# Performance work log

Measured on AMD Instinct MI355X. Metric: run time of the kernel, lower is better.

## Reference

```python
import jax, jax.numpy as jnp
import numpy as np
import math

VOCAB = 50257
BLOCK = 2048
NE = 768


def setup_inputs() -> dict:
    key = jax.random.key(0)
    ks = jax.random.split(key, 12)
    s = 0.02
    idx = jax.random.randint(ks[0], (4, 2048), 0, VOCAB, dtype=jnp.int64 if jax.config.jax_enable_x64 else jnp.int32)
    tok_emb = jax.random.normal(ks[1], (VOCAB, NE), jnp.float32) * s
    pos_emb = jax.random.normal(ks[2], (BLOCK, NE), jnp.float32) * s
    Wk = jax.random.normal(ks[3], (NE, NE), jnp.float32) * s
    bk = jnp.zeros((NE,), jnp.float32)
    Wq = jax.random.normal(ks[4], (NE, NE), jnp.float32) * s
    bq = jnp.zeros((NE,), jnp.float32)
    Wv = jax.random.normal(ks[5], (NE, NE), jnp.float32) * s
    bv = jnp.zeros((NE,), jnp.float32)
    ln_g = jnp.ones((NE,), jnp.float32)
    ln_b = jnp.zeros((NE,), jnp.float32)
    Wh = jax.random.normal(ks[6], (NE, VOCAB), jnp.float32) * s
    bh = jnp.zeros((VOCAB,), jnp.float32)
    return {"idx": idx, "tok_emb": tok_emb, "pos_emb": pos_emb, "Wq": Wq, "bq": bq,
            "Wk": Wk, "bk": bk, "Wv": Wv, "bv": bv, "ln_g": ln_g, "ln_b": ln_b,
            "Wh": Wh, "bh": bh}


def reference(idx, tok_emb, pos_emb, Wq, bq, Wk, bk, Wv, bv, ln_g, ln_b, Wh, bh):
    B, T = idx.shape
    C = tok_emb.shape[1]
    x = tok_emb[idx] + pos_emb[:T]  # [B,T,C]
    q = jnp.einsum('btc,cd->btd', x, Wq) + bq
    k = jnp.einsum('btc,cd->btd', x, Wk) + bk
    v = jnp.einsum('btc,cd->btd', x, Wv) + bv
    att = jnp.einsum('btd,bsd->bts', q, k) / math.sqrt(C)  # [B,T,T]
    causal = jnp.tril(jnp.ones((T, T), bool))
    att = jnp.where(causal, att, -jnp.inf)
    att = jax.nn.softmax(att, axis=-1)
    y = jnp.einsum('bts,bsd->btd', att, v)
    # LayerNorm (eps=1e-5, torch default)
    mu = jnp.mean(y, axis=-1, keepdims=True)
    var = jnp.mean((y - mu) ** 2, axis=-1, keepdims=True)
    yn = (y - mu) * jax.lax.rsqrt(var + 1e-5) * ln_g + ln_b
    logits = jnp.einsum('btc,cv->btv', yn, Wh) + bh
    return logits
```

## Files before the change

kernel.cpp:

```cpp
#include <hip/hip_runtime.h>
#include <hip/hip_bf16.h>
#include <math.h>

typedef __bf16 bf16x8 __attribute__((ext_vector_type(8)));
typedef float  f32x4  __attribute__((ext_vector_type(4)));

#define GAS(p) ((const __attribute__((address_space(1))) void*)(p))
#define LAS(p) ((__attribute__((address_space(3))) void*)(p))

static constexpr int NE = 768;

__global__ __launch_bounds__(256) void k_embed(const int* __restrict__ idx,
    const float* __restrict__ tok, const float* __restrict__ pos,
    __hip_bfloat16* __restrict__ xb)
{
    int bt = blockIdx.x;
    int t  = bt & 2047;
    int token = idx[bt];
    const float* te = tok + (size_t)token * NE;
    const float* pe = pos + (size_t)t * NE;
    __hip_bfloat16* o = xb + (size_t)bt * NE;
    for (int c = threadIdx.x; c < NE; c += 256)
        o[c] = __float2bfloat16(te[c] + pe[c]);
}

__global__ __launch_bounds__(256) void k_transpose_f32_bf16(
    const float* __restrict__ in, __hip_bfloat16* __restrict__ out,
    int R, int C, int outRows)
{
    __shared__ float tile[32][33];
    int c0 = blockIdx.x * 32, r0 = blockIdx.y * 32;
    int tx = threadIdx.x & 31, ty = threadIdx.x >> 5;
    #pragma unroll
    for (int i = 0; i < 32; i += 8) {
        int r = r0 + ty + i, c = c0 + tx;
        tile[ty + i][tx] = (r < R && c < C) ? in[(size_t)r * C + c] : 0.f;
    }
    __syncthreads();
    #pragma unroll
    for (int i = 0; i < 32; i += 8) {
        int oc = c0 + ty + i, orr = r0 + tx;
        if (oc < outRows && orr < R)
            out[(size_t)oc * R + orr] = __float2bfloat16(tile[tx][ty + i]);
    }
}

__global__ __launch_bounds__(256) void k_transpose_bf16(
    const __hip_bfloat16* __restrict__ in, __hip_bfloat16* __restrict__ out,
    int R, int C)
{
    __shared__ __hip_bfloat16 tile[32][33];
    size_t boff = (size_t)blockIdx.z * R * C;
    int c0 = blockIdx.x * 32, r0 = blockIdx.y * 32;
    int tx = threadIdx.x & 31, ty = threadIdx.x >> 5;
    #pragma unroll
    for (int i = 0; i < 32; i += 8)
        tile[ty + i][tx] = in[boff + (size_t)(r0 + ty + i) * C + (c0 + tx)];
    __syncthreads();
    #pragma unroll
    for (int i = 0; i < 32; i += 8)
        out[boff + (size_t)(c0 + ty + i) * R + (r0 + tx)] = tile[tx][ty + i];
}

__global__ __launch_bounds__(256) void k_pack_bias(const float* __restrict__ bq,
    const float* __restrict__ bk, const float* __restrict__ bv, float* __restrict__ o)
{
    int i = blockIdx.x * 256 + threadIdx.x;
    if (i < 768) o[i] = bq[i];
    else if (i < 1536) o[i] = bk[i - 768];
    else if (i < 2304) o[i] = bv[i - 1536];
}

template<int MODE>
__global__ __launch_bounds__(256) void k_gemm(
    const __hip_bfloat16* __restrict__ A, const __hip_bfloat16* __restrict__ Bt,
    int K, int lda, int ldb,
    size_t strideA, size_t strideB, size_t strideC,
    float* __restrict__ outf, int ldc, int ncols,
    const float* __restrict__ bias, float scale,
    __hip_bfloat16* __restrict__ oq, __hip_bfloat16* __restrict__ ok,
    __hip_bfloat16* __restrict__ ov)
{
    int bn = blockIdx.x, bm = blockIdx.y, bz = blockIdx.z;
    if constexpr (MODE == 2) bm = (int)gridDim.y - 1 - bm;
    if (MODE == 1 && bn > bm) return;
    __shared__ __align__(16) __hip_bfloat16 As[128 * 32];
    __shared__ __align__(16) __hip_bfloat16 Bs[128 * 32];
    const __hip_bfloat16* Ab = A  + bz * strideA + (size_t)bm * 128 * lda;
    const __hip_bfloat16* Bb = Bt + bz * strideB + (size_t)bn * 128 * ldb;
    int tid = threadIdx.x, w = tid >> 6, lane = tid & 63;
    int wr = w >> 1, wc = w & 1;
    f32x4 acc[4][4] = {};
    int sr = tid >> 2, sc = (tid & 3) * 8;
    int lr = lane & 15, lk = (lane >> 4) * 8;

    const int kend = (MODE == 2) ? (bm + 1) * 128 : K;

    for (int k0 = 0; k0 < kend; k0 += 32) {
        __syncthreads();
        #pragma unroll
        for (int i = 0; i < 2; ++i) {
            __builtin_amdgcn_global_load_lds(GAS(Ab + (size_t)(i * 64 + sr) * lda + k0 + sc),
                                             LAS((char*)As + i * 4096 + w * 1024), 16, 0, 0);
            __builtin_amdgcn_global_load_lds(GAS(Bb + (size_t)(i * 64 + sr) * ldb + k0 + sc),
                                             LAS((char*)Bs + i * 4096 + w * 1024), 16, 0, 0);
        }
        __syncthreads();
        bf16x8 af[4], bfv[4];
        #pragma unroll
        for (int mi = 0; mi < 4; ++mi)
            af[mi] = *(const bf16x8*)(As + (wr * 64 + mi * 16 + lr) * 32 + lk);
        #pragma unroll
        for (int ni = 0; ni < 4; ++ni)
            bfv[ni] = *(const bf16x8*)(Bs + (wc * 64 + ni * 16 + lr) * 32 + lk);
        #pragma unroll
        for (int mi = 0; mi < 4; ++mi)
            #pragma unroll
            for (int ni = 0; ni < 4; ++ni)
                acc[mi][ni] = __builtin_amdgcn_mfma_f32_16x16x32_bf16(af[mi], bfv[ni], acc[mi][ni], 0, 0, 0);
    }

    int r4 = (lane >> 4) * 4;
    #pragma unroll
    for (int mi = 0; mi < 4; ++mi) {
        #pragma unroll
        for (int ni = 0; ni < 4; ++ni) {
            #pragma unroll
            for (int r = 0; r < 4; ++r) {
                int row = bm * 128 + wr * 64 + mi * 16 + r4 + r;
                int col = bn * 128 + wc * 64 + ni * 16 + lr;
                float v = acc[mi][ni][r];
                if constexpr (MODE == 0) {
                    v += bias[col];
                    __hip_bfloat16 h = __float2bfloat16(v);
                    if (col < 768)       oq[(size_t)row * 768 + col]          = h;
                    else if (col < 1536) ok[(size_t)row * 768 + (col - 768)]  = h;
                    else                 ov[(size_t)row * 768 + (col - 1536)] = h;
                } else if constexpr (MODE == 1) {
                    outf[bz * strideC + (size_t)row * ldc + col] = v * scale;
                } else {
                    outf[bz * strideC + (size_t)row * ldc + col] = v;
                }
            }
        }
    }
}

__global__ __launch_bounds__(512, 2) void k_gemm_head(
    const __hip_bfloat16* __restrict__ A,
    const __hip_bfloat16* __restrict__ Bt,
    float* __restrict__ out, const float* __restrict__ bias, int ldc, int ncols)
{
    constexpr int K = 768, NT = K / 64;
    __shared__ __align__(16) __hip_bfloat16 As[2][256 * 64];
    __shared__ __align__(16) __hip_bfloat16 Bs[2][256 * 64];

    const int bm = blockIdx.x, bn = blockIdx.y;
    const int tid = threadIdx.x;
    const int w = tid >> 6, lane = tid & 63;
    const int wr = w >> 2, wc = w & 3;
    const int lr = lane & 15, lu = lane >> 4;
    const int rswz = lr & 7;

    const int srow = tid >> 3;
    const int sunit = (tid & 7) ^ (srow & 7);
    const size_t Abase = (size_t)bm * 256 * K;
    const size_t Bbase = (size_t)bn * 256 * K;

    auto stageA = [&](int kt, int c, int p) {
        const __hip_bfloat16* src = A + Abase + (size_t)(c * 64 + srow) * K + kt * 64 + sunit * 8;
        __builtin_amdgcn_global_load_lds(GAS(src), LAS(&As[p][c * 4096 + tid * 8]), 16, 0, 0);
    };
    auto stageB = [&](int kt, int c, int p) {
        const __hip_bfloat16* src = Bt + Bbase + (size_t)(c * 64 + srow) * K + kt * 64 + sunit * 8;
        __builtin_amdgcn_global_load_lds(GAS(src), LAS(&Bs[p][c * 4096 + tid * 8]), 16, 0, 0);
    };
    auto rdA = [&](int p, int m, int kk) {
        return *(const bf16x8*)&As[p][(wr * 128 + m * 16 + lr) * 64 + ((kk * 4 + lu) ^ rswz) * 8];
    };
    auto rdB = [&](int p, int n, int kk) {
        return *(const bf16x8*)&Bs[p][(wc * 64 + n * 16 + lr) * 64 + ((kk * 4 + lu) ^ rswz) * 8];
    };

    f32x4 acc[8][4] = {};

    stageB(0, 0, 0); stageB(0, 1, 0); stageB(0, 2, 0); stageB(0, 3, 0);
    stageA(0, 0, 0); stageA(0, 1, 0); stageA(0, 2, 0); stageA(0, 3, 0);
    stageB(1, 0, 1); stageB(1, 1, 1); stageB(1, 2, 1); stageB(1, 3, 1);
    stageA(1, 0, 1); stageA(1, 2, 1);

#define QUAD(Q)                                                                                          \
    {   bf16x8 a00 = rdA(p, 2*(Q),     0), a01 = rdA(p, 2*(Q),     1);                                   \
        bf16x8 a10 = rdA(p, 2*(Q) + 1, 0), a11 = rdA(p, 2*(Q) + 1, 1);                                   \
        __builtin_amdgcn_s_setprio(1);                                                                   \
        _Pragma("unroll")                                                                                \
        for (int n = 0; n < 4; ++n) {                                                                    \
            acc[2*(Q)][n]     = __builtin_amdgcn_mfma_f32_16x16x32_bf16(a00, bf[n][0], acc[2*(Q)][n],     0, 0, 0); \
            acc[2*(Q) + 1][n] = __builtin_amdgcn_mfma_f32_16x16x32_bf16(a10, bf[n][0], acc[2*(Q) + 1][n], 0, 0, 0); \
        }                                                                                                \
        _Pragma("unroll")                                                                                \
        for (int n = 0; n < 4; ++n) {                                                                    \
            acc[2*(Q)][n]     = __builtin_amdgcn_mfma_f32_16x16x32_bf16(a01, bf[n][1], acc[2*(Q)][n],     0, 0, 0); \
            acc[2*(Q) + 1][n] = __builtin_amdgcn_mfma_f32_16x16x32_bf16(a11, bf[n][1], acc[2*(Q) + 1][n], 0, 0, 0); \
        }                                                                                                \
        __builtin_amdgcn_s_setprio(0); }

    for (int kt = 0; kt < NT; ++kt) {
        const int p = kt & 1, pn = p ^ 1;
        if (kt + 1 < NT) {
            stageA(kt + 1, 1, pn); stageA(kt + 1, 3, pn);
            asm volatile("s_waitcnt vmcnt(8)" ::: "memory");
        } else {
            asm volatile("s_waitcnt vmcnt(0)" ::: "memory");
        }
        asm volatile("s_barrier" ::: "memory");
        bf16x8 bf[4][2];
        #pragma unroll
        for (int n = 0; n < 4; ++n) { bf[n][0] = rdB(p, n, 0); bf[n][1] = rdB(p, n, 1); }
        QUAD(0)
        asm volatile("s_barrier" ::: "memory");
        if (kt + 2 < NT) { stageB(kt + 2, 0, p); stageB(kt + 2, 1, p); }
        QUAD(1)
        asm volatile("s_barrier" ::: "memory");
        if (kt + 2 < NT) { stageB(kt + 2, 2, p); stageB(kt + 2, 3, p); }
        QUAD(2)
        asm volatile("s_barrier" ::: "memory");
        if (kt + 2 < NT) { stageA(kt + 2, 0, p); stageA(kt + 2, 2, p); }
        QUAD(3)
        asm volatile("s_barrier" ::: "memory");
    }
#undef QUAD

    const int r4 = lu * 4;
    #pragma unroll
    for (int m = 0; m < 8; ++m) {
        #pragma unroll
        for (int n = 0; n < 4; ++n) {
            int col = bn * 256 + wc * 64 + n * 16 + lr;
            if (col < ncols) {
                float bv_ = bias[col];
                #pragma unroll
                for (int r = 0; r < 4; ++r) {
                    int row = bm * 256 + wr * 128 + m * 16 + r4 + r;
                    out[(size_t)row * ldc + col] = acc[m][n][r] + bv_;
                }
            }
        }
    }
}

__global__ __launch_bounds__(256) void k_softmax(const float* __restrict__ att,
    __hip_bfloat16* __restrict__ P, int T)
{
    int t = blockIdx.x, b = blockIdx.y;
    const float* row = att + ((size_t)b * T + t) * T;
    __hip_bfloat16* prow = P + ((size_t)b * T + t) * T;
    const int n = t + 1;
    const int nz = ((t >> 7) + 1) << 7;
    __shared__ float red[256];
    float4 v[2];
    float mx = -1e30f;
    #pragma unroll
    for (int j = 0; j < 2; ++j) {
        int e = (threadIdx.x + j * 256) * 4;
        v[j] = *(const float4*)(row + e);
        #pragma unroll
        for (int k = 0; k < 4; ++k)
            if (e + k < n) mx = fmaxf(mx, ((const float*)&v[j])[k]);
    }
    red[threadIdx.x] = mx; __syncthreads();
    for (int o = 128; o > 0; o >>= 1) {
        if (threadIdx.x < o) red[threadIdx.x] = fmaxf(red[threadIdx.x], red[threadIdx.x + o]);
        __syncthreads();
    }
    mx = red[0]; __syncthreads();
    float ev[8];
    float sum = 0.f;
    #pragma unroll
    for (int j = 0; j < 2; ++j) {
        int e = (threadIdx.x + j * 256) * 4;
        #pragma unroll
        for (int k = 0; k < 4; ++k) {
            float x = ((const float*)&v[j])[k];
            float ex = (e + k < n) ? __expf(x - mx) : 0.f;
            ev[j * 4 + k] = ex;
            sum += ex;
        }
    }
    red[threadIdx.x] = sum; __syncthreads();
    for (int o = 128; o > 0; o >>= 1) {
        if (threadIdx.x < o) red[threadIdx.x] += red[threadIdx.x + o];
        __syncthreads();
    }
    float inv = 1.f / red[0];
    #pragma unroll
    for (int j = 0; j < 2; ++j) {
        int e = (threadIdx.x + j * 256) * 4;
        #pragma unroll
        for (int k = 0; k < 4; ++k)
            if (e + k < nz) prow[e + k] = __float2bfloat16(ev[j * 4 + k] * inv);
    }
}

__global__ __launch_bounds__(256) void k_layernorm(const float* __restrict__ y,
    const float* __restrict__ g, const float* __restrict__ b,
    __hip_bfloat16* __restrict__ yn)
{
    int row = blockIdx.x;
    const float* yr = y + (size_t)row * NE;
    float s = 0.f, s2 = 0.f;
    for (int c = threadIdx.x; c < NE; c += 256) { float v = yr[c]; s += v; s2 += v * v; }
    __shared__ float r1[256], r2[256];
    r1[threadIdx.x] = s; r2[threadIdx.x] = s2; __syncthreads();
    for (int o = 128; o > 0; o >>= 1) {
        if (threadIdx.x < o) { r1[threadIdx.x] += r1[threadIdx.x + o]; r2[threadIdx.x] += r2[threadIdx.x + o]; }
        __syncthreads();
    }
    float mu = r1[0] / NE;
    float var = r2[0] / NE - mu * mu;
    float rs = rsqrtf(var + 1e-5f);
    __hip_bfloat16* o = yn + (size_t)row * NE;
    for (int c = threadIdx.x; c < NE; c += 256)
        o[c] = __float2bfloat16((yr[c] - mu) * rs * g[c] + b[c]);
}

extern "C" void kernel_launch(void* const* d_in, const int* in_sizes, int n_in,
                              void* d_out, int out_size, void* d_ws, size_t ws_size,
                              hipStream_t stream)
{
    const int*   idx  = (const int*)  d_in[0];
    const float* tok  = (const float*)d_in[1];
    const float* pos  = (const float*)d_in[2];
    const float* Wq   = (const float*)d_in[3];
    const float* bq   = (const float*)d_in[4];
    const float* Wk   = (const float*)d_in[5];
    const float* bk   = (const float*)d_in[6];
    const float* Wv   = (const float*)d_in[7];
    const float* bv   = (const float*)d_in[8];
    const float* ln_g = (const float*)d_in[9];
    const float* ln_b = (const float*)d_in[10];
    const float* Wh   = (const float*)d_in[11];
    const float* bh   = (const float*)d_in[12];
    float* out = (float*)d_out;

    const int B = 4, T = 2048, C = 768, V = 50257, Vp = 50432;

    char* p = (char*)d_ws;
    auto take = [&](size_t bytes) { char* r = p; p += (bytes + 255) & ~(size_t)255; return r; };
    __hip_bfloat16* xb    = (__hip_bfloat16*)take((size_t)B * T * C * 2);
    __hip_bfloat16* wqkvT = (__hip_bfloat16*)take((size_t)3 * C * C * 2);
    float*          bqkv  = (float*)take((size_t)3 * C * 4);
    __hip_bfloat16* qb    = (__hip_bfloat16*)take((size_t)B * T * C * 2);
    __hip_bfloat16* kb    = (__hip_bfloat16*)take((size_t)B * T * C * 2);
    __hip_bfloat16* vb    = (__hip_bfloat16*)take((size_t)B * T * C * 2);
    __hip_bfloat16* vT    = (__hip_bfloat16*)take((size_t)B * T * C * 2);
    float*          att   = (float*)take((size_t)B * T * T * 4);
    __hip_bfloat16* P     = (__hip_bfloat16*)take((size_t)B * T * T * 2);
    float*          y     = (float*)take((size_t)B * T * C * 4);
    __hip_bfloat16* yn    = (__hip_bfloat16*)take((size_t)B * T * C * 2);
    __hip_bfloat16* whT   = (__hip_bfloat16*)att;

    float scale = 1.0f / sqrtf((float)C);

    k_embed<<<dim3(B * T), 256, 0, stream>>>(idx, tok, pos, xb);
    k_transpose_f32_bf16<<<dim3(24, 24), 256, 0, stream>>>(Wq, wqkvT,             C, C, C);
    k_transpose_f32_bf16<<<dim3(24, 24), 256, 0, stream>>>(Wk, wqkvT + C * C,     C, C, C);
    k_transpose_f32_bf16<<<dim3(24, 24), 256, 0, stream>>>(Wv, wqkvT + 2 * C * C, C, C, C);
    k_pack_bias<<<dim3(9), 256, 0, stream>>>(bq, bk, bv, bqkv);

    k_gemm<0><<<dim3(18, 64, 1), 256, 0, stream>>>(xb, wqkvT, C, C, C, 0, 0, 0,
        nullptr, 0, 0, bqkv, 1.f, qb, kb, vb);

    k_transpose_bf16<<<dim3(24, 64, B), 256, 0, stream>>>(vb, vT, T, C);

    k_gemm<1><<<dim3(16, 16, B), 256, 0, stream>>>(qb, kb, C, C, C,
        (size_t)T * C, (size_t)T * C, (size_t)T * T, att, T, 0, nullptr, scale,
        nullptr, nullptr, nullptr);

    k_softmax<<<dim3(T, B), 256, 0, stream>>>(att, P, T);

    k_gemm<2><<<dim3(6, 16, B), 256, 0, stream>>>(P, vT, T, T, T,
        (size_t)T * T, (size_t)C * T, (size_t)T * C, y, C, 0, nullptr, 1.f,
        nullptr, nullptr, nullptr);

    k_transpose_f32_bf16<<<dim3(Vp / 32, 24), 256, 0, stream>>>(Wh, whT, C, V, Vp);

    k_layernorm<<<dim3(B * T), 256, 0, stream>>>(y, ln_g, ln_b, yn);

    k_gemm_head<<<dim3(32, Vp / 256), 512, 0, stream>>>(yn, whT, out, bh, V, V);
}
```

Before: 1.398 ms.

## Shrink head GEMM tiles and simplify double-buffered pipeline for higher occupancy

Replaces the 256x256, BK=64 head GEMM with a 256x128 tile, BK=32 kernel using a simple double buffer and one barrier per k-step, and raises the launch bound to 4 blocks per CU. LDS use drops sharply, which allows more resident blocks to hide latency. In exchange, each tile reuses data less, there are more barriers per unit of work, and the interleaved staging and priority scheduling of the old kernel are gone.

```diff
diff --git a/kernel.cpp b/kernel.cpp
--- a/kernel.cpp
+++ b/kernel.cpp
@@ -146,102 +146,84 @@
     }
 }
 
-__global__ __launch_bounds__(512, 2) void k_gemm_head(
+__global__ __launch_bounds__(512, 4) void k_gemm_head(
     const __hip_bfloat16* __restrict__ A,
     const __hip_bfloat16* __restrict__ Bt,
     float* __restrict__ out, const float* __restrict__ bias, int ldc, int ncols)
 {
-    constexpr int K = 768, NT = K / 64;
-    __shared__ __align__(16) __hip_bfloat16 As[2][256 * 64];
-    __shared__ __align__(16) __hip_bfloat16 Bs[2][256 * 64];
+    constexpr int K = 768, NT = K / 32;
+    __shared__ __align__(16) __hip_bfloat16 As[2][256 * 32];
+    __shared__ __align__(16) __hip_bfloat16 Bs[2][128 * 32];
 
     const int bm = blockIdx.x, bn = blockIdx.y;
     const int tid = threadIdx.x;
     const int w = tid >> 6, lane = tid & 63;
-    const int wr = w >> 2, wc = w & 3;
+    const int wr = w >> 1, wc = w & 1;
     const int lr = lane & 15, lu = lane >> 4;
-    const int rswz = lr & 7;
-
-    const int srow = tid >> 3;
-    const int sunit = (tid & 7) ^ (srow & 7);
-    const size_t Abase = (size_t)bm * 256 * K;
-    const size_t Bbase = (size_t)bn * 256 * K;
-
-    auto stageA = [&](int kt, int c, int p) {
-        const __hip_bfloat16* src = A + Abase + (size_t)(c * 64 + srow) * K + kt * 64 + sunit * 8;
-        __builtin_amdgcn_global_load_lds(GAS(src), LAS(&As[p][c * 4096 + tid * 8]), 16, 0, 0);
+
+    const __hip_bfloat16* Ap = A  + (size_t)(bm * 256) * K;
+    const __hip_bfloat16* Bp = Bt + (size_t)(bn * 128) * K;
+
+    f32x4 acc[4][4] = {};
+
+    auto stage = [&](int kt, int pb) {
+        #pragma unroll
+        for (int l = 0; l < 2; ++l) {
+            int v = l * 512 + tid;
+            int row = v >> 2, uc = v & 3;
+            int s = (row >> 1) & 3;
+            __builtin_amdgcn_global_load_lds(GAS(Ap + (size_t)row * K + kt * 32 + ((uc ^ s) << 3)),
+                                             LAS(&As[pb][v * 8]), 16, 0, 0);
+        }
+        {
+            int v = tid;
+            int row = v >> 2, uc = v & 3;
+            int s = (row >> 1) & 3;
+            __builtin_amdgcn_global_load_lds(GAS(Bp + (size_t)row * K + kt * 32 + ((uc ^ s) << 3)),
+                                             LAS(&Bs[pb][v * 8]), 16, 0, 0);
+        }
     };
-    auto stageB = [&](int kt, int c, int p) {
-        const __hip_bfloat16* src = Bt + Bbase + (size_t)(c * 64 + srow) * K + kt * 64 + sunit * 8;
-        __builtin_amdgcn_global_load_lds(GAS(src), LAS(&Bs[p][c * 4096 + tid * 8]), 16, 0, 0);
+    auto rdA = [&](int pb, int m) {
+        int row = wr * 64 + m * 16 + lr;
+        int s = (row >> 1) & 3;
+        return *(const bf16x8*)&As[pb][row * 32 + ((lu ^ s) << 3)];
     };
-    auto rdA = [&](int p, int m, int kk) {
-        return *(const bf16x8*)&As[p][(wr * 128 + m * 16 + lr) * 64 + ((kk * 4 + lu) ^ rswz) * 8];
+    auto rdB = [&](int pb, int n) {
+        int row = wc * 64 + n * 16 + lr;
+        int s = (row >> 1) & 3;
+        return *(const bf16x8*)&Bs[pb][row * 32 + ((lu ^ s) << 3)];
     };
-    auto rdB = [&](int p, int n, int kk) {
-        return *(const bf16x8*)&Bs[p][(wc * 64 + n * 16 + lr) * 64 + ((kk * 4 + lu) ^ rswz) * 8];
-    };
-
-    f32x4 acc[8][4] = {};
-
-    stageB(0, 0, 0); stageB(0, 1, 0); stageB(0, 2, 0); stageB(0, 3, 0);
-    stageA(0, 0, 0); stageA(0, 1, 0); stageA(0, 2, 0); stageA(0, 3, 0);
-    stageB(1, 0, 1); stageB(1, 1, 1); stageB(1, 2, 1); stageB(1, 3, 1);
-    stageA(1, 0, 1); stageA(1, 2, 1);
-
-#define QUAD(Q)                                                                                          \
-    {   bf16x8 a00 = rdA(p, 2*(Q),     0), a01 = rdA(p, 2*(Q),     1);                                   \
-        bf16x8 a10 = rdA(p, 2*(Q) + 1, 0), a11 = rdA(p, 2*(Q) + 1, 1);                                   \
-        __builtin_amdgcn_s_setprio(1);                                                                   \
-        _Pragma("unroll")                                                                                \
-        for (int n = 0; n < 4; ++n) {                                                                    \
-            acc[2*(Q)][n]     = __builtin_amdgcn_mfma_f32_16x16x32_bf16(a00, bf[n][0], acc[2*(Q)][n],     0, 0, 0); \
-            acc[2*(Q) + 1][n] = __builtin_amdgcn_mfma_f32_16x16x32_bf16(a10, bf[n][0], acc[2*(Q) + 1][n], 0, 0, 0); \
-        }                                                                                                \
-        _Pragma("unroll")                                                                                \
-        for (int n = 0; n < 4; ++n) {                                                                    \
-            acc[2*(Q)][n]     = __builtin_amdgcn_mfma_f32_16x16x32_bf16(a01, bf[n][1], acc[2*(Q)][n],     0, 0, 0); \
-            acc[2*(Q) + 1][n] = __builtin_amdgcn_mfma_f32_16x16x32_bf16(a11, bf[n][1], acc[2*(Q) + 1][n], 0, 0, 0); \
-        }                                                                                                \
-        __builtin_amdgcn_s_setprio(0); }
+
+    stage(0, 0);
+    __syncthreads();
 
     for (int kt = 0; kt < NT; ++kt) {
-        const int p = kt & 1, pn = p ^ 1;
-        if (kt + 1 < NT) {
-            stageA(kt + 1, 1, pn); stageA(kt + 1, 3, pn);
-            asm volatile("s_waitcnt vmcnt(8)" ::: "memory");
-        } else {
-            asm volatile("s_waitcnt vmcnt(0)" ::: "memory");
-        }
-        asm volatile("s_barrier" ::: "memory");
-        bf16x8 bf[4][2];
-        #pragma unroll
-        for (int n = 0; n < 4; ++n) { bf[n][0] = rdB(p, n, 0); bf[n][1] = rdB(p, n, 1); }
-        QUAD(0)
-        asm volatile("s_barrier" ::: "memory");
-        if (kt + 2 < NT) { stageB(kt + 2, 0, p); stageB(kt + 2, 1, p); }
-        QUAD(1)
-        asm volatile("s_barrier" ::: "memory");
-        if (kt + 2 < NT) { stageB(kt + 2, 2, p); stageB(kt + 2, 3, p); }
-        QUAD(2)
-        asm volatile("s_barrier" ::: "memory");
-        if (kt + 2 < NT) { stageA(kt + 2, 0, p); stageA(kt + 2, 2, p); }
-        QUAD(3)
-        asm volatile("s_barrier" ::: "memory");
-    }
-#undef QUAD
+        const int p = kt & 1;
+        if (kt + 1 < NT) stage(kt + 1, p ^ 1);
+        bf16x8 bfv[4];
+        #pragma unroll
+        for (int n = 0; n < 4; ++n) bfv[n] = rdB(p, n);
+        #pragma unroll
+        for (int m = 0; m < 4; ++m) {
+            bf16x8 a = rdA(p, m);
+            #pragma unroll
+            for (int n = 0; n < 4; ++n)
+                acc[m][n] = __builtin_amdgcn_mfma_f32_16x16x32_bf16(a, bfv[n], acc[m][n], 0, 0, 0);
+        }
+        __syncthreads();
+    }
 
     const int r4 = lu * 4;
     #pragma unroll
-    for (int m = 0; m < 8; ++m) {
+    for (int m = 0; m < 4; ++m) {
         #pragma unroll
         for (int n = 0; n < 4; ++n) {
-            int col = bn * 256 + wc * 64 + n * 16 + lr;
+            int col = bn * 128 + wc * 64 + n * 16 + lr;
             if (col < ncols) {
                 float bv_ = bias[col];
                 #pragma unroll
                 for (int r = 0; r < 4; ++r) {
-                    int row = bm * 256 + wr * 128 + m * 16 + r4 + r;
+                    int row = bm * 256 + wr * 64 + m * 16 + r4 + r;
                     out[(size_t)row * ldc + col] = acc[m][n][r] + bv_;
                 }
             }
@@ -387,5 +369,5 @@
 
     k_layernorm<<<dim3(B * T), 256, 0, stream>>>(y, ln_g, ln_b, yn);
 
-    k_gemm_head<<<dim3(32, Vp / 256), 512, 0, stream>>>(yn, whT, out, bh, V, V);
-}
+    k_gemm_head<<<dim3(32, Vp / 128), 512, 0, stream>>>(yn, whT, out, bh, V, V);
+}
```

New measurement: 1.361 ms. 2.7% less time.
